# Optimization experiments

Hardware: AMD Instinct MI355X
Metric: run time of the kernel (lower is better)

Reference implementation:

```python
import jax, jax.numpy as jnp
import numpy as np

STATE_LEN = 128

def _layernorm(x, eps=1e-5):
    m = jnp.mean(x, axis=-1, keepdims=True)
    v = jnp.mean(jnp.square(x - m), axis=-1, keepdims=True)
    return (x - m) * jax.lax.rsqrt(v + eps)

def setup_inputs() -> dict:
    key = jax.random.key(0)
    ks = jax.random.split(key, 20)
    B, S, L = 2, 2048, STATE_LEN
    Din, Dk, Dv, H = 1024, 64, 64, 8
    T = S + 2 * L  # 2304
    x = jax.random.normal(ks[0], (B, T, Din), jnp.float32)
    def w(k, dout):
        return jax.random.normal(k, (H, Din, dout), jnp.float32) / np.sqrt(Din).astype(np.float32)
    inp = {
        'x': x,
        'ln_g':  1.0 + 0.02 * jax.random.normal(ks[1], (H, Din), jnp.float32),
        'ln_b':  0.02 * jax.random.normal(ks[2], (H, Din), jnp.float32),
        'ln_gs': 1.0 + 0.02 * jax.random.normal(ks[3], (H, Din), jnp.float32),
        'ln_bs': 0.02 * jax.random.normal(ks[4], (H, Din), jnp.float32),
        'ln_ge': 1.0 + 0.02 * jax.random.normal(ks[5], (H, Din), jnp.float32),
        'ln_be': 0.02 * jax.random.normal(ks[6], (H, Din), jnp.float32),
        'Wq':   w(ks[7], Dk),  'Wk':   w(ks[8], Dk),  'Wv':   w(ks[9], Dv),
        'Wq_s': w(ks[10], Dk), 'Wk_s': w(ks[11], Dk), 'Wv_s': w(ks[12], Dv),
        'Wq_e': w(ks[13], Dk), 'Wk_e': w(ks[14], Dk), 'Wv_e': w(ks[15], Dv),
        'offset': 0,
    }
    return inp

def _forward(x, ln_g, ln_b, ln_gs, ln_bs, ln_ge, ln_be,
             Wq, Wk, Wv, Wq_s, Wk_s, Wv_s, Wq_e, Wk_e, Wv_e):
    L = STATE_LEN
    B, T, Din = x.shape
    # extract_state: start state, middle sequence, end state
    xs, xm, xe = x[:, :L], x[:, L:T - L], x[:, T - L:]
    # LayerNorm stats are parameter-free; per-head affine applied after
    ns, nm, ne = _layernorm(xs), _layernorm(xm), _layernorm(xe)
    def aff(n, g, b):  # [B,seg,Din] -> [B,H,seg,Din]
        return n[:, None, :, :] * g[None, :, None, :] + b[None, :, None, :]
    hs, hm, he = aff(ns, ln_gs, ln_bs), aff(nm, ln_g, ln_b), aff(ne, ln_ge, ln_be)
    proj = lambda h, W: jnp.einsum('bhsd,hde->bhse', h, W)
    q = jnp.concatenate([proj(hs, Wq_s), proj(hm, Wq), proj(he, Wq_e)], axis=2)
    k = jnp.concatenate([proj(hs, Wk_s), proj(hm, Wk), proj(he, Wk_e)], axis=2)
    v = jnp.concatenate([proj(hs, Wv_s), proj(hm, Wv), proj(he, Wv_e)], axis=2)
    Dk = q.shape[-1]
    scores = jnp.einsum('bhsd,bhtd->bhst', q, k) / jnp.asarray(np.sqrt(Dk), q.dtype)
    # Faithful to the torch code: a FLOAT tril-of-ones mask is passed to SDPA,
    # which ADDS it to the scores (it does not set -inf anywhere).
    mask = jnp.tril(jnp.ones((T, T), scores.dtype))
    att = jax.nn.softmax(scores + mask, axis=-1)
    out = jnp.einsum('bhst,bhtd->bhsd', att, v)  # [B,H,T,Dv]
    H, Dv = out.shape[1], out.shape[3]
    # torch.concat over heads on last dim
    return out.transpose(0, 2, 1, 3).reshape(B, T, H * Dv)

def reference(x, ln_g, ln_b, ln_gs, ln_bs, ln_ge, ln_be,
              Wq, Wk, Wv, Wq_s, Wk_s, Wv_s, Wq_e, Wk_e, Wv_e, offset):
    # offset unused: position_embedders are None in this configuration
    return _forward(x, ln_g, ln_b, ln_gs, ln_bs, ln_ge, ln_be,
                    Wq, Wk, Wv, Wq_s, Wk_s, Wv_s, Wq_e, Wk_e, Wv_e)
```

## Files before the change

kernel.cpp:

```cpp
#include <hip/hip_runtime.h>

#define TSEQ 2304
#define DIN  1024
#define NH   8
#define DD   64
#define NC   1536
#define MROWS 4608
#define L2E  1.44269504f
#define EF   2.71828183f

typedef __attribute__((ext_vector_type(8))) short bf16x8;
typedef __attribute__((ext_vector_type(4))) float f32x4;
typedef __attribute__((ext_vector_type(4))) unsigned short u16x4;

__device__ __forceinline__ unsigned short f2bf(float f){
    union { float f; unsigned int u; } x; x.f = f;
    unsigned int r = x.u + 0x7FFFu + ((x.u >> 16) & 1u);
    return (unsigned short)(r >> 16);
}

__device__ __forceinline__ float exp2raw(float x){
    float r;
    asm("v_exp_f32 %0, %1" : "=v"(r) : "v"(x));
    return r;
}

__device__ __forceinline__ unsigned int cvtpk(float a, float b){
    unsigned int r;
    asm("v_cvt_pk_bf16_f32 %0, %1, %2" : "=v"(r) : "v"(a), "v"(b));
    return r;
}

__device__ __forceinline__ void gload_lds16(const void* g, void* l){
    __builtin_amdgcn_global_load_lds(
        (const __attribute__((address_space(1))) void*)g,
        (__attribute__((address_space(3))) void*)l, 16, 0, 0);
}

struct WArgs {
    const float* W[9];
    const float* g[3];
    const float* bv[3];
};

__global__ __launch_bounds__(256) void k_pre(WArgs a, const float* __restrict__ x,
                                             unsigned short* __restrict__ wb,
                                             float* __restrict__ bias,
                                             unsigned short* __restrict__ nrm)
{
    __shared__ float lds[64][65];
    __shared__ float red[4][64];
    __shared__ float r1[4], r2[4];
    const int bid = blockIdx.x;
    const int tid = threadIdx.x;
    if (bid < 1152){
        const int dt = bid & 15, h = (bid >> 4) & 7, sp = bid >> 7;
        const int seg = sp / 3, proj = sp % 3;
        const float* W = a.W[seg*3 + proj];
        const float* g = a.g[seg];
        const int d0 = dt * 64;
        {
            const int e = tid & 63, rq = tid >> 6;
#pragma unroll
            for (int rr = 0; rr < 16; ++rr){
                const int dl = rr*4 + rq;
                lds[dl][e] = W[((size_t)h*DIN + d0 + dl)*DD + e];
            }
        }
        __syncthreads();
        {
            const int dl = tid & 63, eq = tid >> 6;
            const int n0 = proj*512 + h*64;
            const float gv = g[h*DIN + d0 + dl];
#pragma unroll
            for (int rr = 0; rr < 16; ++rr){
                const int el = eq*16 + rr;
                wb[((size_t)seg*NC + n0 + el)*DIN + d0 + dl] = f2bf(lds[dl][el] * gv);
            }
        }
    } else if (bid < 1224){
        const int u = bid - 1152;
        const int h = u & 7, sp = u >> 3;
        const int seg = sp / 3, proj = sp % 3;
        const float* W  = a.W[seg*3 + proj];
        const float* bv = a.bv[seg];
        const int e = tid & 63, dc = tid >> 6;
        float sum = 0.f;
        for (int i = 0; i < 256; ++i){
            const int d = dc*256 + i;
            sum += bv[h*DIN + d] * W[((size_t)h*DIN + d)*DD + e];
        }
        red[dc][e] = sum;
        __syncthreads();
        if (dc == 0)
            bias[seg*NC + proj*512 + h*64 + e] = red[0][e] + red[1][e] + red[2][e] + red[3][e];
    } else {
        const int row = bid - 1224;
        const float* xr = x + (size_t)row * DIN;
        f32x4 v = *(const f32x4*)&xr[tid*4];
        float s1 = v[0]+v[1]+v[2]+v[3];
        float s2 = v[0]*v[0]+v[1]*v[1]+v[2]*v[2]+v[3]*v[3];
#pragma unroll
        for (int m = 1; m < 64; m <<= 1){ s1 += __shfl_xor(s1, m); s2 += __shfl_xor(s2, m); }
        const int wid = tid >> 6;
        if ((tid & 63) == 0){ r1[wid] = s1; r2[wid] = s2; }
        __syncthreads();
        s1 = r1[0]+r1[1]+r1[2]+r1[3];
        s2 = r2[0]+r2[1]+r2[2]+r2[3];
        const float mean = s1 * (1.f/1024.f);
        const float var  = s2 * (1.f/1024.f) - mean*mean;
        const float rstd = rsqrtf(var + 1e-5f);
        u16x4 ov;
#pragma unroll
        for (int j = 0; j < 4; ++j) ov[j] = f2bf((v[j]-mean)*rstd);
        *(u16x4*)&nrm[(size_t)row*DIN + tid*4] = ov;
    }
}

__global__ __launch_bounds__(256) void k_gemm(
    const unsigned short* __restrict__ A,
    const unsigned short* __restrict__ Wb,
    const float* __restrict__ bias,
    unsigned short* __restrict__ qo,
    unsigned short* __restrict__ ko,
    unsigned short* __restrict__ vt)
{
    __shared__ unsigned short As[128*32];
    __shared__ unsigned short Bs[128*32];
    const int mt = blockIdx.x, nt = blockIdx.y;
    const int row0 = mt*128, n0 = nt*128;
    const int rloc = row0 % TSEQ;
    const int seg = (rloc < 128) ? 0 : (rloc < 2176 ? 1 : 2);
    const unsigned short* Bp = Wb + (size_t)seg * NC * DIN;
    const int tid = threadIdx.x;
    const int wid = tid >> 6, lane = tid & 63;
    const int wr = wid >> 1, wc = wid & 1;
    const int lr = lane & 15, lg = lane >> 4;
    const int srow = lane >> 2;
    const int selem = (lane & 3) * 8;
    f32x4 acc[4][4];
#pragma unroll
    for (int m = 0; m < 4; ++m)
#pragma unroll
        for (int n = 0; n < 4; ++n) acc[m][n] = (f32x4){0.f,0.f,0.f,0.f};

    for (int kt = 0; kt < DIN/32; ++kt){
        const int k0 = kt*32;
        __syncthreads();
#pragma unroll
        for (int i = 0; i < 2; ++i){
            const int c = wid*2 + i;
            const int r = c*16 + srow;
            gload_lds16(&A [(size_t)(row0 + r)*DIN + k0 + selem], &As[c*512]);
            gload_lds16(&Bp[(size_t)(n0  + r)*DIN + k0 + selem], &Bs[c*512]);
        }
        __syncthreads();
        bf16x8 af[4], bfr[4];
#pragma unroll
        for (int m = 0; m < 4; ++m) af[m]  = *(const bf16x8*)&As[(wr*64 + m*16 + lr)*32 + lg*8];
#pragma unroll
        for (int n = 0; n < 4; ++n) bfr[n] = *(const bf16x8*)&Bs[(wc*64 + n*16 + lr)*32 + lg*8];
#pragma unroll
        for (int m = 0; m < 4; ++m)
#pragma unroll
            for (int n = 0; n < 4; ++n)
                acc[m][n] = __builtin_amdgcn_mfma_f32_16x16x32_bf16(af[m], bfr[n], acc[m][n], 0, 0, 0);
    }
    const int b_ = row0 / TSEQ;
    const int t0 = row0 - b_ * TSEQ;
#pragma unroll
    for (int m = 0; m < 4; ++m){
#pragma unroll
        for (int n = 0; n < 4; ++n){
            const int nglob = n0 + wc*64 + n*16 + lr;
            const float bs = bias[seg*NC + nglob];
            const int proj = nglob >> 9, hh = (nglob >> 6) & 7, e = nglob & 63;
            if (proj < 2){
                unsigned short* op = (proj == 0) ? qo : ko;
                const float scale = (proj == 0) ? 0.125f * L2E : 1.0f;
                const size_t ob = ((size_t)(b_*NH + hh) * TSEQ) * DD + e;
#pragma unroll
                for (int j = 0; j < 4; ++j){
                    const int t = t0 + wr*64 + m*16 + 4*lg + j;
                    op[ob + (size_t)t * DD] = f2bf((acc[m][n][j] + bs) * scale);
                }
            } else {
                unsigned short* vp = vt + ((size_t)(b_*NH + hh)*DD + e)*TSEQ;
                const int t = t0 + wr*64 + m*16 + 4*lg;
                u16x4 pk;
#pragma unroll
                for (int j = 0; j < 4; ++j) pk[j] = f2bf(acc[m][n][j] + bs);
                *(u16x4*)&vp[t] = pk;
            }
        }
    }
}

__global__ __launch_bounds__(256) void k_attn(
    const unsigned short* __restrict__ Q,
    const unsigned short* __restrict__ K,
    const unsigned short* __restrict__ Vt,
    float* __restrict__ po0,
    float* __restrict__ po1,
    float* __restrict__ out2,
    float* __restrict__ pl)
{
    __shared__ unsigned short Ks[2][64*64];
    __shared__ unsigned short Vs[2][64*64];
    __shared__ unsigned short Plds[4][32][72];
    const int qtb = blockIdx.x;
    const int bh  = blockIdx.y;
    const int z   = blockIdx.z;
    const int kt0 = z*12, kt1 = kt0 + 12;
    const int tid  = threadIdx.x;
    const int w    = tid >> 6;
    const int lane = tid & 63;
    const int lr = lane & 15, lg = lane >> 4;
    const size_t qkb = (size_t)bh * TSEQ * DD;
    const size_t vtb = (size_t)bh * DD * TSEQ;
    const int q0w = qtb*128 + w*32;
    const int kd  = qtb*2 + (w >> 1);

    const int rsub = lane >> 3;
    const int cgx  = (lane & 7) ^ rsub;
    const char* Kbase  = (const char*)(K  + qkb);
    const char* Vtbase = (const char*)(Vt + vtb);

    bf16x8 aq[2][2];
#pragma unroll
    for (int qg = 0; qg < 2; ++qg)
#pragma unroll
        for (int ks = 0; ks < 2; ++ks)
            aq[qg][ks] = *(const bf16x8*)&Q[qkb + (size_t)(q0w + qg*16 + lr)*DD + ks*32 + lg*8];

    float lsum[2] = {0.f, 0.f};
    f32x4 o[2][4];
#pragma unroll
    for (int qg = 0; qg < 2; ++qg)
#pragma unroll
        for (int nd = 0; nd < 4; ++nd) o[qg][nd] = (f32x4){0.f,0.f,0.f,0.f};

    auto stage = [&](int kt, int b){
        const int kn = kt*64;
#pragma unroll
        for (int i = 0; i < 2; ++i){
            const int c = w*2 + i;
            const int r = c*8 + rsub;
            gload_lds16(Kbase  + (size_t)(kn + r)*128 + cgx*16,              &Ks[b][c*512]);
            gload_lds16(Vtbase + (size_t)r*(TSEQ*2) + (size_t)kn*2 + cgx*16, &Vs[b][c*512]);
        }
    };

    stage(kt0, 0);
    __syncthreads();

    unsigned int* PldsW = (unsigned int*)&Plds[w][0][0];

    int buf = 0;
    for (int kt = kt0; kt < kt1; ++kt){
        const int kc0 = kt*64;
        if (kt + 1 < kt1) stage(kt + 1, buf ^ 1);
        bf16x8 bk[2][4];
#pragma unroll
        for (int ks = 0; ks < 2; ++ks)
#pragma unroll
            for (int ns = 0; ns < 4; ++ns)
                bk[ks][ns] = *(const bf16x8*)&Ks[buf][(ns*16 + lr)*64 + (((4*ks + lg) ^ (lr & 7))*8)];
        f32x4 s[2][4];
#pragma unroll
        for (int qg = 0; qg < 2; ++qg)
#pragma unroll
            for (int ns = 0; ns < 4; ++ns) s[qg][ns] = (f32x4){0.f,0.f,0.f,0.f};
#pragma unroll
        for (int qg = 0; qg < 2; ++qg)
#pragma unroll
            for (int ks = 0; ks < 2; ++ks)
#pragma unroll
                for (int ns = 0; ns < 4; ++ns)
                    s[qg][ns] = __builtin_amdgcn_mfma_f32_16x16x32_bf16(bk[ks][ns], aq[qg][ks], s[qg][ns], 0, 0, 0);
        if (kt == kd){
#pragma unroll
            for (int qg = 0; qg < 2; ++qg){
                lsum[qg] *= EF;
#pragma unroll
                for (int nd = 0; nd < 4; ++nd)
#pragma unroll
                    for (int j = 0; j < 4; ++j) o[qg][nd][j] *= EF;
                const int qr = q0w + qg*16 + lr;
#pragma unroll
                for (int ns = 0; ns < 4; ++ns){
                    const int kb = kc0 + ns*16 + 4*lg;
                    float p0 = exp2raw(s[qg][ns][0] + ((kb + 0 <= qr) ? L2E : 0.f));
                    float p1 = exp2raw(s[qg][ns][1] + ((kb + 1 <= qr) ? L2E : 0.f));
                    float p2 = exp2raw(s[qg][ns][2] + ((kb + 2 <= qr) ? L2E : 0.f));
                    float p3 = exp2raw(s[qg][ns][3] + ((kb + 3 <= qr) ? L2E : 0.f));
                    lsum[qg] += (p0 + p1) + (p2 + p3);
                    PldsW[(qg*16 + lr)*36 + ns*8 + 2*lg + 0] = cvtpk(p0, p1);
                    PldsW[(qg*16 + lr)*36 + ns*8 + 2*lg + 1] = cvtpk(p2, p3);
                }
            }
        } else {
#pragma unroll
            for (int qg = 0; qg < 2; ++qg){
#pragma unroll
                for (int ns = 0; ns < 4; ++ns){
                    float p0 = exp2raw(s[qg][ns][0]);
                    float p1 = exp2raw(s[qg][ns][1]);
                    float p2 = exp2raw(s[qg][ns][2]);
                    float p3 = exp2raw(s[qg][ns][3]);
                    lsum[qg] += (p0 + p1) + (p2 + p3);
                    PldsW[(qg*16 + lr)*36 + ns*8 + 2*lg + 0] = cvtpk(p0, p1);
                    PldsW[(qg*16 + lr)*36 + ns*8 + 2*lg + 1] = cvtpk(p2, p3);
                }
            }
        }
        bf16x8 bv[2][4];
#pragma unroll
        for (int ks = 0; ks < 2; ++ks)
#pragma unroll
            for (int nd = 0; nd < 4; ++nd)
                bv[ks][nd] = *(const bf16x8*)&Vs[buf][(nd*16 + lr)*64 + (((4*ks + lg) ^ (lr & 7))*8)];
#pragma unroll
        for (int qg = 0; qg < 2; ++qg){
            bf16x8 pa0 = *(const bf16x8*)&Plds[w][qg*16 + lr][0*32 + lg*8];
            bf16x8 pa1 = *(const bf16x8*)&Plds[w][qg*16 + lr][1*32 + lg*8];
#pragma unroll
            for (int nd = 0; nd < 4; ++nd){
                o[qg][nd] = __builtin_amdgcn_mfma_f32_16x16x32_bf16(pa0, bv[0][nd], o[qg][nd], 0, 0, 0);
                o[qg][nd] = __builtin_amdgcn_mfma_f32_16x16x32_bf16(pa1, bv[1][nd], o[qg][nd], 0, 0, 0);
            }
        }
        __syncthreads();
        buf ^= 1;
    }
    if (kd >= kt1){
#pragma unroll
        for (int qg = 0; qg < 2; ++qg){
            lsum[qg] *= EF;
#pragma unroll
            for (int nd = 0; nd < 4; ++nd)
#pragma unroll
                for (int j = 0; j < 4; ++j) o[qg][nd][j] *= EF;
        }
    }
#pragma unroll
    for (int qg = 0; qg < 2; ++qg){
        lsum[qg] += __shfl_xor(lsum[qg], 16);
        lsum[qg] += __shfl_xor(lsum[qg], 32);
    }
    const int pbase = ((z*16 + bh)*18 + qtb)*128 + w*32;
    if (lg == 0){
        pl[pbase + 0*16 + lr] = lsum[0];
        pl[pbase + 1*16 + lr] = lsum[1];
    }
    if (z < 2){
        float* po = (z == 0) ? po0 : po1;
        const size_t tb = ((size_t)(bh*18 + qtb)*128 + w*32) * 64;
#pragma unroll
        for (int qg = 0; qg < 2; ++qg)
#pragma unroll
            for (int j = 0; j < 4; ++j)
#pragma unroll
                for (int nd = 0; nd < 4; ++nd)
                    po[tb + (size_t)(qg*16 + 4*lg + j)*64 + nd*16 + lr] = o[qg][nd][j];
    } else {
        const int b_ = bh >> 3, hh = bh & 7;
#pragma unroll
        for (int qg = 0; qg < 2; ++qg){
#pragma unroll
            for (int j = 0; j < 4; ++j){
                const int t = q0w + qg*16 + 4*lg + j;
                const size_t ob = ((size_t)(b_*TSEQ + t))*512 + hh*64;
#pragma unroll
                for (int nd = 0; nd < 4; ++nd)
                    out2[ob + nd*16 + lr] = o[qg][nd][j];
            }
        }
    }
}

__global__ __launch_bounds__(256) void k_comb(
    const float* __restrict__ po0, const float* __restrict__ po1,
    const float* __restrict__ pl, float* __restrict__ out)
{
    const int qt = blockIdx.x, bh = blockIdx.y;
    const int b_ = bh >> 3, hh = bh & 7;
    const int tid = threadIdx.x;
    const int row = tid >> 2;
    const int c0  = (tid & 3) * 16;
    const int t128  = qt >> 1;
    const int rowin = (qt & 1)*64 + row;
    const int plb = (bh*18 + t128)*128 + rowin;
    const float inv = 1.0f / (pl[plb] + pl[(16*18*128) + plb] + pl[(2*16*18*128) + plb]);
    const size_t tb = ((size_t)(bh*18 + t128)*128 + rowin)*64 + c0;
    const size_t ob = ((size_t)(b_*TSEQ + qt*64 + row))*512 + hh*64 + c0;
#pragma unroll
    for (int i = 0; i < 4; ++i){
        f32x4 a = *(const f32x4*)&po0[tb + i*4];
        f32x4 b = *(const f32x4*)&po1[tb + i*4];
        f32x4 c = *(const f32x4*)&out[ob + i*4];
        f32x4 r;
#pragma unroll
        for (int j = 0; j < 4; ++j) r[j] = (a[j] + b[j] + c[j]) * inv;
        *(f32x4*)&out[ob + i*4] = r;
    }
}

extern "C" void kernel_launch(void* const* d_in, const int* in_sizes, int n_in,
                              void* d_out, int out_size, void* d_ws, size_t ws_size,
                              hipStream_t stream)
{
    const float* x     = (const float*)d_in[0];
    const float* ln_g  = (const float*)d_in[1];
    const float* ln_b  = (const float*)d_in[2];
    const float* ln_gs = (const float*)d_in[3];
    const float* ln_bs = (const float*)d_in[4];
    const float* ln_ge = (const float*)d_in[5];
    const float* ln_be = (const float*)d_in[6];
    const float* Wq    = (const float*)d_in[7];
    const float* Wk    = (const float*)d_in[8];
    const float* Wv    = (const float*)d_in[9];
    const float* Wq_s  = (const float*)d_in[10];
    const float* Wk_s  = (const float*)d_in[11];
    const float* Wv_s  = (const float*)d_in[12];
    const float* Wq_e  = (const float*)d_in[13];
    const float* Wk_e  = (const float*)d_in[14];
    const float* Wv_e  = (const float*)d_in[15];

    uint8_t* w = (uint8_t*)d_ws;
    unsigned short* nrm = (unsigned short*)(w);
    unsigned short* wb  = (unsigned short*)(w + 9437184);
    float*          bia = (float*)        (w + 18874368);
    unsigned short* q_  = (unsigned short*)(w + 18892800);
    unsigned short* k_  = (unsigned short*)(w + 23611392);
    unsigned short* vt_ = (unsigned short*)(w + 28329984);
    float*          pl  = (float*)        (w + 33048576);
    float*          po0 = (float*)        (w);
    float*          po1 = (float*)        (w + 9437184);

    WArgs wa;
    wa.W[0] = Wq_s; wa.W[1] = Wk_s; wa.W[2] = Wv_s;
    wa.W[3] = Wq;   wa.W[4] = Wk;   wa.W[5] = Wv;
    wa.W[6] = Wq_e; wa.W[7] = Wk_e; wa.W[8] = Wv_e;
    wa.g[0] = ln_gs; wa.g[1] = ln_g; wa.g[2] = ln_ge;
    wa.bv[0] = ln_bs; wa.bv[1] = ln_b; wa.bv[2] = ln_be;

    float* out = (float*)d_out;
    k_pre <<<dim3(5832),      dim3(256), 0, stream>>>(wa, x, wb, bia, nrm);
    k_gemm<<<dim3(36, 12),    dim3(256), 0, stream>>>(nrm, wb, bia, q_, k_, vt_);
    k_attn<<<dim3(18, 16, 3), dim3(256), 0, stream>>>(q_, k_, vt_, po0, po1, out, pl);
    k_comb<<<dim3(36, 16),    dim3(256), 0, stream>>>(po0, po1, pl, out);
}
```

Before: 102.0 us.

## Replace LDS round-trip for P with ds_bpermute register shuffles in attention

Converts the softmax probability tile from the S accumulator layout into the MFMA A-operand layout using ds_bpermute lane shuffles instead of writing it to and reading it back from a per-wave LDS buffer. This drops the Plds shared array, which reduces LDS footprint, and adds a launch-bounds hint of 4 blocks per CU to raise occupancy. It also interleaves the K fragment loads with the QK MFMAs and hoists the V loads ahead of the softmax. In exchange it issues 16 bpermutes per qg per tile plus selects, and the occupancy hint may force register spills.

```diff
diff --git a/kernel.cpp b/kernel.cpp
--- a/kernel.cpp
+++ b/kernel.cpp
@@ -12,6 +12,7 @@
 typedef __attribute__((ext_vector_type(8))) short bf16x8;
 typedef __attribute__((ext_vector_type(4))) float f32x4;
 typedef __attribute__((ext_vector_type(4))) unsigned short u16x4;
+typedef __attribute__((ext_vector_type(4))) unsigned int u32x4;
 
 __device__ __forceinline__ unsigned short f2bf(float f){
     union { float f; unsigned int u; } x; x.f = f;
@@ -196,7 +197,7 @@
     }
 }
 
-__global__ __launch_bounds__(256) void k_attn(
+__global__ __launch_bounds__(256, 4) void k_attn(
     const unsigned short* __restrict__ Q,
     const unsigned short* __restrict__ K,
     const unsigned short* __restrict__ Vt,
@@ -207,7 +208,6 @@
 {
     __shared__ unsigned short Ks[2][64*64];
     __shared__ unsigned short Vs[2][64*64];
-    __shared__ unsigned short Plds[4][32][72];
     const int qtb = blockIdx.x;
     const int bh  = blockIdx.y;
     const int z   = blockIdx.z;
@@ -226,6 +226,10 @@
     const char* Kbase  = (const char*)(K  + qkb);
     const char* Vtbase = (const char*)(Vt + vtb);
 
+    const int sl0 = (lr + ((lg & 1) << 5)) * 4;
+    const int sl1 = sl0 + 64;
+    const bool hi = (lg >> 1) != 0;
+
     bf16x8 aq[2][2];
 #pragma unroll
     for (int qg = 0; qg < 2; ++qg)
@@ -254,33 +258,34 @@
     stage(kt0, 0);
     __syncthreads();
 
-    unsigned int* PldsW = (unsigned int*)&Plds[w][0][0];
-
     int buf = 0;
     for (int kt = kt0; kt < kt1; ++kt){
         const int kc0 = kt*64;
         if (kt + 1 < kt1) stage(kt + 1, buf ^ 1);
-        bf16x8 bk[2][4];
+        f32x4 s[2][4];
+#pragma unroll
+        for (int qg = 0; qg < 2; ++qg)
+#pragma unroll
+            for (int ns = 0; ns < 4; ++ns) s[qg][ns] = (f32x4){0.f,0.f,0.f,0.f};
 #pragma unroll
         for (int ks = 0; ks < 2; ++ks)
 #pragma unroll
-            for (int ns = 0; ns < 4; ++ns)
-                bk[ks][ns] = *(const bf16x8*)&Ks[buf][(ns*16 + lr)*64 + (((4*ks + lg) ^ (lr & 7))*8)];
-        f32x4 s[2][4];
-#pragma unroll
-        for (int qg = 0; qg < 2; ++qg)
-#pragma unroll
-            for (int ns = 0; ns < 4; ++ns) s[qg][ns] = (f32x4){0.f,0.f,0.f,0.f};
-#pragma unroll
-        for (int qg = 0; qg < 2; ++qg)
-#pragma unroll
-            for (int ks = 0; ks < 2; ++ks)
-#pragma unroll
-                for (int ns = 0; ns < 4; ++ns)
-                    s[qg][ns] = __builtin_amdgcn_mfma_f32_16x16x32_bf16(bk[ks][ns], aq[qg][ks], s[qg][ns], 0, 0, 0);
-        if (kt == kd){
-#pragma unroll
-            for (int qg = 0; qg < 2; ++qg){
+            for (int ns = 0; ns < 4; ++ns){
+                bf16x8 bk = *(const bf16x8*)&Ks[buf][(ns*16 + lr)*64 + (((4*ks + lg) ^ (lr & 7))*8)];
+#pragma unroll
+                for (int qg = 0; qg < 2; ++qg)
+                    s[qg][ns] = __builtin_amdgcn_mfma_f32_16x16x32_bf16(bk, aq[qg][ks], s[qg][ns], 0, 0, 0);
+            }
+        bf16x8 bv[2][4];
+#pragma unroll
+        for (int ks = 0; ks < 2; ++ks)
+#pragma unroll
+            for (int nd = 0; nd < 4; ++nd)
+                bv[ks][nd] = *(const bf16x8*)&Vs[buf][(nd*16 + lr)*64 + (((4*ks + lg) ^ (lr & 7))*8)];
+#pragma unroll
+        for (int qg = 0; qg < 2; ++qg){
+            unsigned int u_[4][2];
+            if (kt == kd){
                 lsum[qg] *= EF;
 #pragma unroll
                 for (int nd = 0; nd < 4; ++nd)
@@ -295,13 +300,10 @@
                     float p2 = exp2raw(s[qg][ns][2] + ((kb + 2 <= qr) ? L2E : 0.f));
                     float p3 = exp2raw(s[qg][ns][3] + ((kb + 3 <= qr) ? L2E : 0.f));
                     lsum[qg] += (p0 + p1) + (p2 + p3);
-                    PldsW[(qg*16 + lr)*36 + ns*8 + 2*lg + 0] = cvtpk(p0, p1);
-                    PldsW[(qg*16 + lr)*36 + ns*8 + 2*lg + 1] = cvtpk(p2, p3);
+                    u_[ns][0] = cvtpk(p0, p1);
+                    u_[ns][1] = cvtpk(p2, p3);
                 }
-            }
-        } else {
-#pragma unroll
-            for (int qg = 0; qg < 2; ++qg){
+            } else {
 #pragma unroll
                 for (int ns = 0; ns < 4; ++ns){
                     float p0 = exp2raw(s[qg][ns][0]);
@@ -309,25 +311,31 @@
                     float p2 = exp2raw(s[qg][ns][2]);
                     float p3 = exp2raw(s[qg][ns][3]);
                     lsum[qg] += (p0 + p1) + (p2 + p3);
-                    PldsW[(qg*16 + lr)*36 + ns*8 + 2*lg + 0] = cvtpk(p0, p1);
-                    PldsW[(qg*16 + lr)*36 + ns*8 + 2*lg + 1] = cvtpk(p2, p3);
+                    u_[ns][0] = cvtpk(p0, p1);
+                    u_[ns][1] = cvtpk(p2, p3);
                 }
             }
-        }
-        bf16x8 bv[2][4];
-#pragma unroll
-        for (int ks = 0; ks < 2; ++ks)
-#pragma unroll
-            for (int nd = 0; nd < 4; ++nd)
-                bv[ks][nd] = *(const bf16x8*)&Vs[buf][(nd*16 + lr)*64 + (((4*ks + lg) ^ (lr & 7))*8)];
-#pragma unroll
-        for (int qg = 0; qg < 2; ++qg){
-            bf16x8 pa0 = *(const bf16x8*)&Plds[w][qg*16 + lr][0*32 + lg*8];
-            bf16x8 pa1 = *(const bf16x8*)&Plds[w][qg*16 + lr][1*32 + lg*8];
-#pragma unroll
-            for (int nd = 0; nd < 4; ++nd){
-                o[qg][nd] = __builtin_amdgcn_mfma_f32_16x16x32_bf16(pa0, bv[0][nd], o[qg][nd], 0, 0, 0);
-                o[qg][nd] = __builtin_amdgcn_mfma_f32_16x16x32_bf16(pa1, bv[1][nd], o[qg][nd], 0, 0, 0);
+#pragma unroll
+            for (int ks = 0; ks < 2; ++ks){
+                u32x4 wv;
+                {
+                    unsigned int a0 = (unsigned int)__builtin_amdgcn_ds_bpermute(sl0, (int)u_[2*ks+0][0]);
+                    unsigned int b0 = (unsigned int)__builtin_amdgcn_ds_bpermute(sl0, (int)u_[2*ks+1][0]);
+                    wv[0] = hi ? b0 : a0;
+                    unsigned int a1 = (unsigned int)__builtin_amdgcn_ds_bpermute(sl0, (int)u_[2*ks+0][1]);
+                    unsigned int b1 = (unsigned int)__builtin_amdgcn_ds_bpermute(sl0, (int)u_[2*ks+1][1]);
+                    wv[1] = hi ? b1 : a1;
+                    unsigned int a2 = (unsigned int)__builtin_amdgcn_ds_bpermute(sl1, (int)u_[2*ks+0][0]);
+                    unsigned int b2 = (unsigned int)__builtin_amdgcn_ds_bpermute(sl1, (int)u_[2*ks+1][0]);
+                    wv[2] = hi ? b2 : a2;
+                    unsigned int a3 = (unsigned int)__builtin_amdgcn_ds_bpermute(sl1, (int)u_[2*ks+0][1]);
+                    unsigned int b3 = (unsigned int)__builtin_amdgcn_ds_bpermute(sl1, (int)u_[2*ks+1][1]);
+                    wv[3] = hi ? b3 : a3;
+                }
+                bf16x8 pa = __builtin_bit_cast(bf16x8, wv);
+#pragma unroll
+                for (int nd = 0; nd < 4; ++nd)
+                    o[qg][nd] = __builtin_amdgcn_mfma_f32_16x16x32_bf16(pa, bv[ks][nd], o[qg][nd], 0, 0, 0);
             }
         }
         __syncthreads();
```

After: 117.4 us. 15.1% more time.
